# Performance work log

Hardware: AMD Instinct MI355X
Metric: run time of the kernel (lower is better)

## Reference

```python
import jax, jax.numpy as jnp
import numpy as np

BS, RAL, LAL = 64, 2048, 250
CS, VOC, HFS, EMB = 256, 34, 512, 256


def _lstm_cell(x, h, c, Wih, Whh, bih, bhh):
    # torch.nn.LSTMCell gate order: i, f, g, o
    gates = x @ Wih.T + bih + h @ Whh.T + bhh
    i, f, g, o = jnp.split(gates, 4, axis=-1)
    c_new = jax.nn.sigmoid(f) * c + jax.nn.sigmoid(i) * jnp.tanh(g)
    h_new = jax.nn.sigmoid(o) * jnp.tanh(c_new)
    return h_new, c_new


def setup_inputs() -> dict:
    k0 = jax.random.key(0)
    ks = jax.random.split(k0, 20)
    s = 0.05
    inp = {
        'key': jax.random.normal(ks[0], (BS, RAL, CS), jnp.float32),
        'val': jax.random.normal(ks[1], (BS, RAL, CS), jnp.float32),
        'y': jax.random.randint(ks[2], (BS, LAL), 0, VOC, jnp.int64),
        'mask': jnp.ones((BS, RAL), jnp.float32),
        'emb_table': jax.random.normal(ks[3], (VOC, EMB), jnp.float32) * s,
        'Wih_a': jax.random.normal(ks[4], (4 * HFS, EMB + CS), jnp.float32) * s,
        'Whh_a': jax.random.normal(ks[5], (4 * HFS, HFS), jnp.float32) * s,
        'bih_a': jnp.zeros((4 * HFS,), jnp.float32),
        'bhh_a': jnp.zeros((4 * HFS,), jnp.float32),
        'Wih_b': jax.random.normal(ks[6], (4 * HFS, HFS), jnp.float32) * s,
        'Whh_b': jax.random.normal(ks[7], (4 * HFS, HFS), jnp.float32) * s,
        'bih_b': jnp.zeros((4 * HFS,), jnp.float32),
        'bhh_b': jnp.zeros((4 * HFS,), jnp.float32),
        'Wq': jax.random.normal(ks[8], (CS, HFS), jnp.float32) * s,
        'bq': jnp.zeros((CS,), jnp.float32),
        'Wc': jax.random.normal(ks[9], (VOC, HFS + CS), jnp.float32) * s,
        'bc': jnp.zeros((VOC,), jnp.float32),
    }
    return inp


def reference(key, val, mask, emb_table, Wih_a, Whh_a, bih_a, bhh_a,
              Wih_b, Whh_b, bih_b, bhh_b, Wq, bq, Wc, bc, y):
    bs = key.shape[0]
    emb_seq = emb_table[y]                       # (BS, LAL, EMB)
    emb_seq = jnp.swapaxes(emb_seq, 0, 1)        # (LAL, BS, EMB)
    neg = jnp.asarray(-1e9, key.dtype)
    valid = mask > 0                             # (BS, RAL)

    h_a0 = jnp.zeros((bs, HFS), key.dtype)
    init = (h_a0, h_a0, h_a0, h_a0, jnp.zeros((bs, CS), key.dtype))

    def step(carry, emb_t):
        h_a, c_a, h_b, c_b, context = carry
        lstm_in = jnp.concatenate([emb_t, context], axis=1)      # (BS, EMB+CS)
        h_a, c_a = _lstm_cell(lstm_in, h_a, c_a, Wih_a, Whh_a, bih_a, bhh_a)
        h_b, c_b = _lstm_cell(h_a, h_b, c_b, Wih_b, Whh_b, bih_b, bhh_b)
        query = h_b @ Wq.T + bq                                  # (BS, CS)
        energy = jnp.einsum('brc,bc->br', key, query)            # (BS, RAL)
        energy = jnp.where(valid, energy, neg)
        attention = jax.nn.softmax(energy, axis=-1)
        context = jnp.einsum('br,brc->bc', attention, val)       # (BS, CS)
        y_next = jnp.concatenate([h_b, context], axis=1) @ Wc.T + bc  # (BS, VOC)
        return (h_a, c_a, h_b, c_b, context), y_next

    _, pred = jax.lax.scan(step, init, emb_seq)  # (LAL, BS, VOC)
    return jnp.swapaxes(pred, 0, 1)              # (BS, LAL, VOC)
```

## Files before the change

kernel.cpp:

```cpp
#include <hip/hip_runtime.h>

typedef _Float16 h2 __attribute__((ext_vector_type(2)));
typedef _Float16 h4 __attribute__((ext_vector_type(4)));
typedef _Float16 h8 __attribute__((ext_vector_type(8)));
union H8 { h8 v; h2 p[4]; };

#define AGENT __HIP_MEMORY_SCOPE_AGENT
#define NT 1024

__device__ __forceinline__ float dot2(h2 a, h2 b, float c) {
#if __has_builtin(__builtin_amdgcn_fdot2)
  return __builtin_amdgcn_fdot2(a, b, c, false);
#else
  return c + (float)a[0]*(float)b[0] + (float)a[1]*(float)b[1];
#endif
}
__device__ __forceinline__ float dot8(h8 x, h8 w, float acc) {
  H8 a, b; a.v = x; b.v = w;
  acc = dot2(a.p[0], b.p[0], acc); acc = dot2(a.p[1], b.p[1], acc);
  acc = dot2(a.p[2], b.p[2], acc); acc = dot2(a.p[3], b.p[3], acc);
  return acc;
}
__device__ __forceinline__ float sigm(float x){ return 1.f/(1.f+__expf(-x)); }

enum : unsigned long long {
  OFF_CA   = 4096ull,
  OFF_CB   = 135168ull,
  OFF_HA   = 266240ull,
  OFF_HB   = 397312ull,
  OFF_CTX  = 528384ull,
  ZERO_W32 = 140288ull,
  OFF_PART = 561152ull,
  OFF_PEMB = 839680ull,
  OFF_BB   = 1118208ull,
  OFF_FLAG = 1126400ull,
  OFF_WA   = 1126656ull,
  OFF_WB   = 4272384ull,
  OFF_WQ   = 8466688ull,
  OFF_WC   = 8728832ull,
  OFF_K16  = 8782080ull,
  OFF_V16  = 75890944ull,
  TOTAL_FULL = 142999808ull
};

#define S3_HBS  0
#define S3_QH   1536
#define S3_PL   2048
#define S3_RED  4096
#define S3_YRED 36864
#define S3_SCAL 38016
#define EX_OFF  132096
#define YS_OFF  136192
#define SMEM_BYTES 136448

struct P {
  const float *key, *val, *mask, *bq, *bc;
  const void* y;
  const _Float16 *k16, *v16;
  float *Pemb, *bb;
  _Float16 *Wa, *Wb, *Wq, *Wc;
  float *ca, *cb, *parts;
  _Float16 *ha, *hb, *ctx;
  unsigned *gctr, *grel, *qctr;
  const int* flag;
  float* out;
};

__device__ __forceinline__ void gsync(unsigned* ctr, unsigned* rel, int e) {
  __syncthreads();
  if (threadIdx.x == 0) {
    __threadfence();
    unsigned a = __hip_atomic_fetch_add(ctr, 1u, __ATOMIC_RELAXED, AGENT);
    if (a == (unsigned)(e*256 - 1)) {
      __hip_atomic_store(rel, (unsigned)e, __ATOMIC_RELEASE, AGENT);
    } else {
      while (__hip_atomic_load(rel, __ATOMIC_RELAXED, AGENT) < (unsigned)e)
        __builtin_amdgcn_s_sleep(2);
    }
    __threadfence();
  }
  __syncthreads();
}

template<int K, bool YS>
__device__ __forceinline__ void lstm_phase(char* sm, int wg, int tid,
    const _Float16* src0, int len0, const _Float16* src1,
    const _Float16* Wcat, const float* accInit,
    const void* yv, int yIs64, int t,
    float* cSt, _Float16* hOut)
{
  constexpr int SK = K/8;
  const int S0 = len0/8;
  h8* xs = (h8*)sm;
  int* ysL = (int*)(sm + YS_OFF);
  if (YS && tid < 64) {
    long idx = (long)tid*250 + t;
    ysL[tid] = yIs64 ? (int)((const long long*)yv)[idx] : ((const int*)yv)[idx];
  }
  for (int i = tid; i < 64*SK; i += NT) {
    int b_ = i / SK, k8 = i % SK;
    const _Float16* s = (k8 < S0) ? (src0 + b_*len0 + k8*8)
                                  : (src1 + b_*512 + (k8 - S0)*8);
    xs[b_*(SK+1) + k8] = *(const h8*)s;
  }
  __syncthreads();
  const int b = tid & 63, rs = tid >> 6;
  const int jj = rs & 1, g = (rs >> 1) & 3, s = rs >> 3;
  const int n = g*512 + wg*2 + jj;
  float acc = 0.f;
  const h8* wrow = (const h8*)(Wcat + (size_t)n*K);
  const h8* xrow = xs + b*(SK+1);
  #pragma unroll 8
  for (int m = 0; m < SK/2; ++m) acc = dot8(xrow[2*m+s], wrow[2*m+s], acc);
  float* ex = (float*)(sm + EX_OFF);
  ex[rs*64 + b] = acc;
  __syncthreads();
  if (tid < 128) {
    int j2 = tid >> 6, b2 = tid & 63;
    int n0 = wg*2 + j2;
    float i0, i1, i2, i3;
    if (YS) {
      const float* pe = accInit + (size_t)ysL[b2]*2048 + n0;
      i0 = pe[0]; i1 = pe[512]; i2 = pe[1024]; i3 = pe[1536];
    } else {
      i0 = accInit[n0]; i1 = accInit[512+n0]; i2 = accInit[1024+n0]; i3 = accInit[1536+n0];
    }
    float iv = ex[(0+j2)*64+b2] + ex[(8+0+j2)*64+b2] + i0;
    float fv = ex[(2+j2)*64+b2] + ex[(8+2+j2)*64+b2] + i1;
    float gv = ex[(4+j2)*64+b2] + ex[(8+4+j2)*64+b2] + i2;
    float ov = ex[(6+j2)*64+b2] + ex[(8+6+j2)*64+b2] + i3;
    int ci = b2*512 + wg*2 + j2;
    float cn = sigm(fv)*cSt[ci] + sigm(iv)*tanhf(gv);
    cSt[ci] = cn;
    hOut[ci] = (_Float16)(sigm(ov)*tanhf(cn));
  }
}

template<bool KV16>
__device__ __forceinline__ void attn(char* sm, const P& p, int wg, int tid, int t, int wrB) {
  const int b = wg >> 2, quarter = wg & 3;
  _Float16* hbs = (_Float16*)(sm + S3_HBS);
  _Float16* qh  = (_Float16*)(sm + S3_QH);
  float* pl   = (float*)(sm + S3_PL);
  float* red  = (float*)(sm + S3_RED);
  float* yred = (float*)(sm + S3_YRED);
  float* scal = (float*)(sm + S3_SCAL);
  if (tid < 512) hbs[tid] = p.hb[wrB*32768 + b*512 + tid];
  __syncthreads();
  if (tid < 256) {
    float a = p.bq[tid];
    const h8* wr = (const h8*)(p.Wq + (size_t)tid*512);
    const h8* hx = (const h8*)hbs;
    #pragma unroll 8
    for (int k = 0; k < 64; ++k) a = dot8(hx[k], wr[k], a);
    qh[tid] = (_Float16)a;
  }
  __syncthreads();
  {
    const int l = tid & 63, wv = tid >> 6, lr = l >> 4, lc = l & 15;
    const int rbase = quarter*512 + wv*32 + lr;
    if constexpr (KV16) {
      h2 q2[8];
      const h2* qp = (const h2*)qh;
      #pragma unroll
      for (int j = 0; j < 8; ++j) q2[j] = qp[lc*8 + j];
      const _Float16* kbase = p.k16 + ((size_t)b*2048 + rbase)*256 + lc*16;
      h8 ka[8], kb[8];
      #pragma unroll
      for (int it = 0; it < 8; ++it) {
        const h8* kp = (const h8*)(kbase + (size_t)it*4*256);
        ka[it] = kp[0]; kb[it] = kp[1];
      }
      #pragma unroll
      for (int it = 0; it < 8; ++it) {
        float e = 0.f;
        H8 a0, a1; a0.v = ka[it]; a1.v = kb[it];
        e = dot2(a0.p[0], q2[0], e); e = dot2(a0.p[1], q2[1], e);
        e = dot2(a0.p[2], q2[2], e); e = dot2(a0.p[3], q2[3], e);
        e = dot2(a1.p[0], q2[4], e); e = dot2(a1.p[1], q2[5], e);
        e = dot2(a1.p[2], q2[6], e); e = dot2(a1.p[3], q2[7], e);
        e += __shfl_xor(e, 1); e += __shfl_xor(e, 2);
        e += __shfl_xor(e, 4); e += __shfl_xor(e, 8);
        if (lc == 0) {
          int rl = wv*32 + it*4 + lr;
          pl[rl] = (p.mask[b*2048 + quarter*512 + rl] > 0.f) ? e : -1e9f;
        }
      }
    } else {
      float qf[16];
      #pragma unroll
      for (int j = 0; j < 16; ++j) qf[j] = (float)qh[lc*16 + j];
      const float* kbase = p.key + ((size_t)b*2048 + rbase)*256 + lc*16;
      for (int ii = 0; ii < 4; ++ii) {
        float4 kv[2][4];
        #pragma unroll
        for (int jt = 0; jt < 2; ++jt) {
          const float4* kp = (const float4*)(kbase + (size_t)(ii*2+jt)*4*256);
          #pragma unroll
          for (int j = 0; j < 4; ++j) kv[jt][j] = kp[j];
        }
        #pragma unroll
        for (int jt = 0; jt < 2; ++jt) {
          float e = 0.f;
          #pragma unroll
          for (int j = 0; j < 4; ++j)
            e += kv[jt][j].x*qf[j*4+0] + kv[jt][j].y*qf[j*4+1]
               + kv[jt][j].z*qf[j*4+2] + kv[jt][j].w*qf[j*4+3];
          e += __shfl_xor(e, 1); e += __shfl_xor(e, 2);
          e += __shfl_xor(e, 4); e += __shfl_xor(e, 8);
          if (lc == 0) {
            int rl = wv*32 + (ii*2+jt)*4 + lr;
            pl[rl] = (p.mask[b*2048 + quarter*512 + rl] > 0.f) ? e : -1e9f;
          }
        }
      }
    }
  }
  __syncthreads();
  {
    float v = (tid < 512) ? pl[tid] : -1e30f;
    float m = v;
    #pragma unroll
    for (int s2 = 32; s2; s2 >>= 1) m = fmaxf(m, __shfl_xor(m, s2));
    if (tid < 512 && !(tid & 63)) red[tid >> 6] = m;
    __syncthreads();
    if (!tid) {
      float mm = red[0];
      for (int i = 1; i < 8; ++i) mm = fmaxf(mm, red[i]);
      scal[0] = mm;
    }
    __syncthreads();
    float pe = 0.f;
    if (tid < 512) { pe = __expf(v - scal[0]); pl[tid] = pe; }
    float s = pe;
    #pragma unroll
    for (int s2 = 32; s2; s2 >>= 1) s += __shfl_xor(s, s2);
    if (tid < 512 && !(tid & 63)) red[tid >> 6] = s;
    __syncthreads();
    if (!tid) {
      float ss = 0;
      for (int i = 0; i < 8; ++i) ss += red[i];
      scal[1] = ss;
    }
    __syncthreads();
  }
  {
    const int l32 = tid & 31, rs32 = tid >> 5;
    float a[8] = {0,0,0,0,0,0,0,0};
    if constexpr (KV16) {
      const _Float16* vbase = p.v16 + ((size_t)b*2048 + quarter*512 + rs32*16)*256 + l32*8;
      #pragma unroll
      for (int ii = 0; ii < 2; ++ii) {
        h8 vv[8];
        #pragma unroll
        for (int j = 0; j < 8; ++j) vv[j] = *(const h8*)(vbase + (size_t)(ii*8+j)*256);
        #pragma unroll
        for (int j = 0; j < 8; ++j) {
          float pr = pl[rs32*16 + ii*8 + j];
          #pragma unroll
          for (int c = 0; c < 8; ++c) a[c] += pr * (float)vv[j][c];
        }
      }
    } else {
      const float* vbase = p.val + ((size_t)b*2048 + quarter*512 + rs32*16)*256 + l32*8;
      for (int ii = 0; ii < 4; ++ii) {
        float4 v4[4][2];
        #pragma unroll
        for (int j = 0; j < 4; ++j) {
          const float4* vp = (const float4*)(vbase + (size_t)(ii*4+j)*256);
          v4[j][0] = vp[0]; v4[j][1] = vp[1];
        }
        #pragma unroll
        for (int j = 0; j < 4; ++j) {
          float pr = pl[rs32*16 + ii*4 + j];
          a[0] += pr*v4[j][0].x; a[1] += pr*v4[j][0].y;
          a[2] += pr*v4[j][0].z; a[3] += pr*v4[j][0].w;
          a[4] += pr*v4[j][1].x; a[5] += pr*v4[j][1].y;
          a[6] += pr*v4[j][1].z; a[7] += pr*v4[j][1].w;
        }
      }
    }
    float* rd = red + rs32*256 + l32*8;
    ((float4*)rd)[0] = make_float4(a[0], a[1], a[2], a[3]);
    ((float4*)rd)[1] = make_float4(a[4], a[5], a[6], a[7]);
  }
  __syncthreads();
  if (tid < 256) {
    float s = 0;
    #pragma unroll
    for (int r = 0; r < 32; ++r) s += red[r*256 + tid];
    float* pb = p.parts + (size_t)b*1088 + quarter*272;
    pb[tid] = s;
    if (!tid) { pb[256] = scal[0]; pb[257] = scal[1]; }
  }
  __syncthreads();
  if (!tid) {
    __threadfence();
    __hip_atomic_fetch_add(p.qctr + b, 1u, __ATOMIC_RELAXED, AGENT);
  }
  if (quarter == 0) {
    if (!tid) {
      while (__hip_atomic_load(p.qctr + b, __ATOMIC_RELAXED, AGENT) < 4u*(unsigned)(t+1))
        __builtin_amdgcn_s_sleep(2);
      __threadfence();
    }
    __syncthreads();
    if (tid < 256) {
      const float* pb = p.parts + (size_t)b*1088;
      float m0 = pb[256], s0 = pb[257], m1 = pb[272+256], s1 = pb[272+257];
      float m2 = pb[544+256], s2 = pb[544+257], m3 = pb[816+256], s3 = pb[816+257];
      float M = fmaxf(fmaxf(m0, m1), fmaxf(m2, m3));
      float w0 = __expf(m0-M), w1 = __expf(m1-M), w2 = __expf(m2-M), w3 = __expf(m3-M);
      float S = w0*s0 + w1*s1 + w2*s2 + w3*s3;
      float cv = (w0*pb[tid] + w1*pb[272+tid] + w2*pb[544+tid] + w3*pb[816+tid]) / S;
      hbs[512 + tid] = (_Float16)cv;
      p.ctx[b*256 + tid] = (_Float16)cv;
    }
    __syncthreads();
    {
      int vq = tid >> 3, ks = tid & 7;
      if (vq < 34) {
        float a = 0;
        const h8* wr = (const h8*)(p.Wc + (size_t)vq*768 + ks*96);
        const h8* xx = (const h8*)hbs + ks*12;
        #pragma unroll
        for (int i = 0; i < 12; ++i) a = dot8(xx[i], wr[i], a);
        yred[vq*8 + ks] = a;
      }
    }
    __syncthreads();
    if (tid < 34) {
      float a = p.bc[tid];
      #pragma unroll
      for (int k = 0; k < 8; ++k) a += yred[tid*8 + k];
      p.out[((size_t)b*250 + t)*34 + tid] = a;
    }
  }
}

template<bool KV16>
__global__ __launch_bounds__(NT, 4) void speller_main(P p) {
  __shared__ __align__(16) char sm[SMEM_BYTES];
  const int wg = blockIdx.x, tid = threadIdx.x;
  const int y64 = *p.flag;
  int ep = 0;
  for (int t = 0; t < 250; ++t) {
    const int rd = t & 1, wr = 1 - rd;
    lstm_phase<768, true>(sm, wg, tid, p.ctx, 256, p.ha + rd*32768, p.Wa,
                          p.Pemb, p.y, y64, t, p.ca, p.ha + wr*32768);
    gsync(p.gctr, p.grel, ++ep);
    lstm_phase<1024, false>(sm, wg, tid, p.ha + wr*32768, 512, p.hb + rd*32768, p.Wb,
                            p.bb, nullptr, 0, 0, p.cb, p.hb + wr*32768);
    gsync(p.gctr, p.grel, ++ep);
    attn<KV16>(sm, p, wg, tid, t, wr);
    gsync(p.gctr, p.grel, ++ep);
  }
}

__global__ void prep_a(P p, const float* emb, const float* Wih_a, const float* Whh_a,
    const float* bih_a, const float* bhh_a, const float* Wih_b, const float* Whh_b,
    const float* bih_b, const float* bhh_b, const float* Wqf, const float* Wcf,
    unsigned* zb, int* flag)
{
  int id = blockIdx.x*blockDim.x + threadIdx.x;
  int N = gridDim.x*blockDim.x;
  for (int i = id; i < (int)ZERO_W32; i += N) zb[i] = 0u;
  for (int i = id; i < 34*2048; i += N) {
    int v = i >> 11, n = i & 2047;
    float a = bih_a[n] + bhh_a[n];
    const float4* e4 = (const float4*)(emb + v*256);
    const float4* w4 = (const float4*)(Wih_a + (size_t)n*512);
    for (int k = 0; k < 64; ++k) {
      float4 x = e4[k], w = w4[k];
      a += x.x*w.x + x.y*w.y + x.z*w.z + x.w*w.w;
    }
    p.Pemb[i] = a;
  }
  for (int i = id; i < 2048*768; i += N) {
    int n = i / 768, k = i % 768;
    float w = (k < 256) ? Wih_a[(size_t)n*512 + 256 + k] : Whh_a[(size_t)n*512 + k - 256];
    p.Wa[i] = (_Float16)w;
  }
  for (int i = id; i < 2048*1024; i += N) {
    int n = i >> 10, k = i & 1023;
    float w = (k < 512) ? Wih_b[(size_t)n*512 + k] : Whh_b[(size_t)n*512 + k - 512];
    p.Wb[i] = (_Float16)w;
  }
  for (int i = id; i < 256*512; i += N) p.Wq[i] = (_Float16)Wqf[i];
  for (int i = id; i < 34*768; i += N) p.Wc[i] = (_Float16)Wcf[i];
  for (int i = id; i < 2048; i += N) p.bb[i] = bih_b[i] + bhh_b[i];
  if (id == 0) {
    const long long* yl = (const long long*)p.y;
    int ok = 1;
    for (int i = 0; i < 200; ++i) { long long v = yl[i]; if (v < 0 || v >= 34) { ok = 0; break; } }
    *flag = ok;
  }
}

__global__ void prep_kv(const float* key, const float* val, _Float16* k16, _Float16* v16) {
  int id = blockIdx.x*blockDim.x + threadIdx.x;
  int N = gridDim.x*blockDim.x;
  const int PER = 8388608;
  for (int i = id; i < 2*PER; i += N) {
    const float4* src; _Float16* dst; int j;
    if (i < PER) { src = (const float4*)key; dst = k16; j = i; }
    else         { src = (const float4*)val; dst = v16; j = i - PER; }
    float4 x = src[j];
    h4 o; o[0] = (_Float16)x.x; o[1] = (_Float16)x.y; o[2] = (_Float16)x.z; o[3] = (_Float16)x.w;
    *(h4*)(dst + (size_t)j*4) = o;
  }
}

extern "C" void kernel_launch(void* const* d_in, const int* in_sizes, int n_in,
                              void* d_out, int out_size, void* d_ws, size_t ws_size,
                              hipStream_t stream) {
  char* ws = (char*)d_ws;
  P p;
  p.key = (const float*)d_in[0];
  p.val = (const float*)d_in[1];
  p.y   = d_in[2];
  p.mask = (const float*)d_in[3];
  p.bq = (const float*)d_in[14];
  p.bc = (const float*)d_in[16];
  p.gctr = (unsigned*)(ws + 0);
  p.grel = (unsigned*)(ws + 4);
  p.qctr = (unsigned*)(ws + 256);
  p.ca = (float*)(ws + OFF_CA);
  p.cb = (float*)(ws + OFF_CB);
  p.ha = (_Float16*)(ws + OFF_HA);
  p.hb = (_Float16*)(ws + OFF_HB);
  p.ctx = (_Float16*)(ws + OFF_CTX);
  p.parts = (float*)(ws + OFF_PART);
  p.Pemb = (float*)(ws + OFF_PEMB);
  p.bb = (float*)(ws + OFF_BB);
  p.flag = (const int*)(ws + OFF_FLAG);
  p.Wa = (_Float16*)(ws + OFF_WA);
  p.Wb = (_Float16*)(ws + OFF_WB);
  p.Wq = (_Float16*)(ws + OFF_WQ);
  p.Wc = (_Float16*)(ws + OFF_WC);
  p.k16 = (const _Float16*)(ws + OFF_K16);
  p.v16 = (const _Float16*)(ws + OFF_V16);
  p.out = (float*)d_out;

  bool kv16 = ws_size >= (size_t)TOTAL_FULL;

  prep_a<<<dim3(1024), dim3(256), 0, stream>>>(p,
      (const float*)d_in[4], (const float*)d_in[5], (const float*)d_in[6],
      (const float*)d_in[7], (const float*)d_in[8], (const float*)d_in[9],
      (const float*)d_in[10], (const float*)d_in[11], (const float*)d_in[12],
      (const float*)d_in[13], (const float*)d_in[15],
      (unsigned*)ws, (int*)(ws + OFF_FLAG));
  if (kv16) {
    prep_kv<<<dim3(4096), dim3(256), 0, stream>>>(p.key, p.val,
        (_Float16*)(ws + OFF_K16), (_Float16*)(ws + OFF_V16));
    speller_main<true><<<dim3(256), dim3(NT), 0, stream>>>(p);
  } else {
    speller_main<false><<<dim3(256), dim3(NT), 0, stream>>>(p);
  }
}
```

Measured before the change: 39.78 ms.

## Replace atomic-counter grid barrier with per-block flags and context-ready flags

Replaces the single-counter fetch-add grid barrier with per-block flag slots, padded to separate cache lines, that block 0 polls before releasing everyone. The third barrier per step is removed and replaced by per-batch context-ready flags that each block waits on at the start of the next step, so blocks only wait for the data they need. The mask is read once into per-thread bitmasks instead of from global memory every step, the LSTM dot-product loop now walks contiguous halves rather than interleaved elements, and launch bounds drop the occupancy hint. These changes target barrier contention and per-step latency, at the cost of centralizing barrier polling in block 0.

```diff
diff --git a/kernel.cpp b/kernel.cpp
--- a/kernel.cpp
+++ b/kernel.cpp
@@ -24,23 +24,26 @@
 __device__ __forceinline__ float sigm(float x){ return 1.f/(1.f+__expf(-x)); }
 
 enum : unsigned long long {
-  OFF_CA   = 4096ull,
-  OFF_CB   = 135168ull,
-  OFF_HA   = 266240ull,
-  OFF_HB   = 397312ull,
-  OFF_CTX  = 528384ull,
-  ZERO_W32 = 140288ull,
-  OFF_PART = 561152ull,
-  OFF_PEMB = 839680ull,
-  OFF_BB   = 1118208ull,
-  OFF_FLAG = 1126400ull,
-  OFF_WA   = 1126656ull,
-  OFF_WB   = 4272384ull,
-  OFF_WQ   = 8466688ull,
-  OFF_WC   = 8728832ull,
-  OFF_K16  = 8782080ull,
-  OFF_V16  = 75890944ull,
-  TOTAL_FULL = 142999808ull
+  OFF_CA    = 4096ull,
+  OFF_CB    = 135168ull,
+  OFF_HA    = 266240ull,
+  OFF_HB    = 397312ull,
+  OFF_CTX   = 528384ull,
+  OFF_FLAGS = 561152ull,
+  OFF_CFLAG = 593920ull,
+  OFF_QCTR  = 602112ull,
+  ZERO_W32  = 152576ull,
+  OFF_PART  = 610304ull,
+  OFF_PEMB  = 888832ull,
+  OFF_BB    = 1167360ull,
+  OFF_FLAG  = 1175552ull,
+  OFF_WA    = 1175808ull,
+  OFF_WB    = 4321536ull,
+  OFF_WQ    = 8515840ull,
+  OFF_WC    = 8777984ull,
+  OFF_K16   = 8830976ull,
+  OFF_V16   = 75939840ull,
+  TOTAL_FULL = 143048704ull
 };
 
 #define S3_HBS  0
@@ -61,22 +64,32 @@
   _Float16 *Wa, *Wb, *Wq, *Wc;
   float *ca, *cb, *parts;
   _Float16 *ha, *hb, *ctx;
-  unsigned *gctr, *grel, *qctr;
+  int *flags, *cflag, *grel;
+  unsigned *qctr;
   const int* flag;
   float* out;
 };
 
-__device__ __forceinline__ void gsync(unsigned* ctr, unsigned* rel, int e) {
-  __syncthreads();
-  if (threadIdx.x == 0) {
+__device__ __forceinline__ void gsync(const P& p, int e) {
+  const int tid = threadIdx.x, wg = blockIdx.x;
+  __syncthreads();
+  if (tid == 0) {
     __threadfence();
-    unsigned a = __hip_atomic_fetch_add(ctr, 1u, __ATOMIC_RELAXED, AGENT);
-    if (a == (unsigned)(e*256 - 1)) {
-      __hip_atomic_store(rel, (unsigned)e, __ATOMIC_RELEASE, AGENT);
-    } else {
-      while (__hip_atomic_load(rel, __ATOMIC_RELAXED, AGENT) < (unsigned)e)
-        __builtin_amdgcn_s_sleep(2);
-    }
+    __hip_atomic_store(p.flags + (size_t)wg*32, e, __ATOMIC_RELEASE, AGENT);
+  }
+  if (wg == 0) {
+    for (;;) {
+      int ok = 1;
+      if (tid < 256) ok = (__hip_atomic_load(p.flags + (size_t)tid*32, __ATOMIC_RELAXED, AGENT) >= e);
+      if (__syncthreads_and(ok)) break;
+    }
+    if (tid == 0) {
+      __threadfence();
+      __hip_atomic_store(p.grel, e, __ATOMIC_RELEASE, AGENT);
+    }
+  } else if (tid == 0) {
+    while (__hip_atomic_load(p.grel, __ATOMIC_RELAXED, AGENT) < e)
+      __builtin_amdgcn_s_sleep(2);
     __threadfence();
   }
   __syncthreads();
@@ -108,10 +121,10 @@
   const int jj = rs & 1, g = (rs >> 1) & 3, s = rs >> 3;
   const int n = g*512 + wg*2 + jj;
   float acc = 0.f;
-  const h8* wrow = (const h8*)(Wcat + (size_t)n*K);
-  const h8* xrow = xs + b*(SK+1);
+  const h8* wrow = (const h8*)(Wcat + (size_t)n*K) + s*(SK/2);
+  const h8* xrow = xs + b*(SK+1) + s*(SK/2);
   #pragma unroll 8
-  for (int m = 0; m < SK/2; ++m) acc = dot8(xrow[2*m+s], wrow[2*m+s], acc);
+  for (int m = 0; m < SK/2; ++m) acc = dot8(xrow[m], wrow[m], acc);
   float* ex = (float*)(sm + EX_OFF);
   ex[rs*64 + b] = acc;
   __syncthreads();
@@ -137,7 +150,8 @@
 }
 
 template<bool KV16>
-__device__ __forceinline__ void attn(char* sm, const P& p, int wg, int tid, int t, int wrB) {
+__device__ __forceinline__ void attn(char* sm, const P& p, int wg, int tid, int t,
+                                     int wrB, unsigned mbits) {
   const int b = wg >> 2, quarter = wg & 3;
   _Float16* hbs = (_Float16*)(sm + S3_HBS);
   _Float16* qh  = (_Float16*)(sm + S3_QH);
@@ -183,7 +197,7 @@
         e += __shfl_xor(e, 4); e += __shfl_xor(e, 8);
         if (lc == 0) {
           int rl = wv*32 + it*4 + lr;
-          pl[rl] = (p.mask[b*2048 + quarter*512 + rl] > 0.f) ? e : -1e9f;
+          pl[rl] = ((mbits >> it) & 1u) ? e : -1e9f;
         }
       }
     } else {
@@ -209,8 +223,9 @@
           e += __shfl_xor(e, 1); e += __shfl_xor(e, 2);
           e += __shfl_xor(e, 4); e += __shfl_xor(e, 8);
           if (lc == 0) {
-            int rl = wv*32 + (ii*2+jt)*4 + lr;
-            pl[rl] = (p.mask[b*2048 + quarter*512 + rl] > 0.f) ? e : -1e9f;
+            int it = ii*2 + jt;
+            int rl = wv*32 + it*4 + lr;
+            pl[rl] = ((mbits >> it) & 1u) ? e : -1e9f;
           }
         }
       }
@@ -296,12 +311,12 @@
   __syncthreads();
   if (!tid) {
     __threadfence();
-    __hip_atomic_fetch_add(p.qctr + b, 1u, __ATOMIC_RELAXED, AGENT);
+    __hip_atomic_fetch_add(p.qctr + (size_t)b*32, 1u, __ATOMIC_RELAXED, AGENT);
   }
   if (quarter == 0) {
     if (!tid) {
-      while (__hip_atomic_load(p.qctr + b, __ATOMIC_RELAXED, AGENT) < 4u*(unsigned)(t+1))
-        __builtin_amdgcn_s_sleep(2);
+      while (__hip_atomic_load(p.qctr + (size_t)b*32, __ATOMIC_RELAXED, AGENT) < 4u*(unsigned)(t+1))
+        __builtin_amdgcn_s_sleep(1);
       __threadfence();
     }
     __syncthreads();
@@ -317,6 +332,10 @@
       p.ctx[b*256 + tid] = (_Float16)cv;
     }
     __syncthreads();
+    if (!tid) {
+      __threadfence();
+      __hip_atomic_store(p.cflag + (size_t)b*32, t + 1, __ATOMIC_RELEASE, AGENT);
+    }
     {
       int vq = tid >> 3, ks = tid & 7;
       if (vq < 34) {
@@ -339,21 +358,40 @@
 }
 
 template<bool KV16>
-__global__ __launch_bounds__(NT, 4) void speller_main(P p) {
+__global__ __launch_bounds__(NT) void speller_main(P p) {
   __shared__ __align__(16) char sm[SMEM_BYTES];
   const int wg = blockIdx.x, tid = threadIdx.x;
   const int y64 = *p.flag;
+  unsigned mbits = 0;
+  {
+    const int b = wg >> 2, quarter = wg & 3;
+    const int l = tid & 63, wv = tid >> 6, lr = l >> 4, lc = l & 15;
+    if (lc == 0) {
+      for (int it = 0; it < 8; ++it) {
+        int rl = wv*32 + it*4 + lr;
+        if (p.mask[b*2048 + quarter*512 + rl] > 0.f) mbits |= (1u << it);
+      }
+    }
+  }
   int ep = 0;
   for (int t = 0; t < 250; ++t) {
     const int rd = t & 1, wr = 1 - rd;
+    {
+      for (;;) {
+        int ok = 1;
+        if (tid < 64) ok = (__hip_atomic_load(p.cflag + (size_t)tid*32, __ATOMIC_RELAXED, AGENT) >= t);
+        if (__syncthreads_and(ok)) break;
+      }
+      if (!tid) __threadfence();
+      __syncthreads();
+    }
     lstm_phase<768, true>(sm, wg, tid, p.ctx, 256, p.ha + rd*32768, p.Wa,
                           p.Pemb, p.y, y64, t, p.ca, p.ha + wr*32768);
-    gsync(p.gctr, p.grel, ++ep);
+    gsync(p, ++ep);
     lstm_phase<1024, false>(sm, wg, tid, p.ha + wr*32768, 512, p.hb + rd*32768, p.Wb,
                             p.bb, nullptr, 0, 0, p.cb, p.hb + wr*32768);
-    gsync(p.gctr, p.grel, ++ep);
-    attn<KV16>(sm, p, wg, tid, t, wr);
-    gsync(p.gctr, p.grel, ++ep);
+    gsync(p, ++ep);
+    attn<KV16>(sm, p, wg, tid, t, wr, mbits);
   }
 }
 
@@ -422,14 +460,15 @@
   p.mask = (const float*)d_in[3];
   p.bq = (const float*)d_in[14];
   p.bc = (const float*)d_in[16];
-  p.gctr = (unsigned*)(ws + 0);
-  p.grel = (unsigned*)(ws + 4);
-  p.qctr = (unsigned*)(ws + 256);
+  p.grel = (int*)(ws + 128);
   p.ca = (float*)(ws + OFF_CA);
   p.cb = (float*)(ws + OFF_CB);
   p.ha = (_Float16*)(ws + OFF_HA);
   p.hb = (_Float16*)(ws + OFF_HB);
   p.ctx = (_Float16*)(ws + OFF_CTX);
+  p.flags = (int*)(ws + OFF_FLAGS);
+  p.cflag = (int*)(ws + OFF_CFLAG);
+  p.qctr = (unsigned*)(ws + OFF_QCTR);
   p.parts = (float*)(ws + OFF_PART);
   p.Pemb = (float*)(ws + OFF_PEMB);
   p.bb = (float*)(ws + OFF_BB);
```

New measurement: 33.37 ms. 1.19x faster.
